# Kernel tuning notes

Hardware: AMD Instinct MI355X
Metric: run time of the kernel (lower is better)

## Reference

```python
import jax, jax.numpy as jnp
import numpy as np

H = 512; W = 512; C = 32; B = 2; N = 120000; HEADS = 2; HD = C // HEADS; S = 9
INDEX_SHIFT = jnp.array([[0,0],[-1,0],[1,0],[0,1],[-1,1],[1,1],[0,-1],[-1,-1],[1,-1]], dtype=jnp.int32)


def setup_inputs() -> dict:
    key = jax.random.key(0)
    ks = jax.random.split(key, 20)
    bev_feats = jax.random.normal(ks[0], (B, N, C), jnp.float32)
    coors = []
    for b in range(B):
        perm = jax.random.permutation(ks[1 + b], H * W)[:N]
        coors.append(jnp.stack([perm // W, perm % W], axis=-1))
    bev_coors = jnp.stack(coors).astype(jnp.int32)
    s = 1.0 / np.sqrt(C)
    u = lambda k, shape, lim: jax.random.uniform(k, shape, jnp.float32, -lim, lim)
    return {
        'bev_feats': bev_feats,
        'bev_coors': bev_coors,
        'ln_w': jnp.ones((C,), jnp.float32),
        'ln_b': jnp.zeros((C,), jnp.float32),
        'wq': u(ks[3], (C, C), s), 'bq': u(ks[4], (C,), s),
        'wk': u(ks[5], (C, C), s), 'bk': u(ks[6], (C,), s),
        'wv': u(ks[7], (C, C), s), 'bv': u(ks[8], (C,), s),
        'pos_w': u(ks[9], (C, 2), 1.0 / np.sqrt(2.0)), 'pos_b': u(ks[10], (C,), 1.0 / np.sqrt(2.0)),
        'in_w': u(ks[11], (3 * C, C), s), 'in_b': jnp.zeros((3 * C,), jnp.float32),
        'out_w': u(ks[12], (C, C), s), 'out_b': jnp.zeros((C,), jnp.float32),
    }


def reference(bev_feats, bev_coors, ln_w, ln_b, wq, bq, wk, bk, wv, bv, pos_w, pos_b, in_w, in_b, out_w, out_b):
    def single(feats, coors):
        # LayerNorm (biased var, eps=1e-5)
        mu = feats.mean(-1, keepdims=True)
        var = feats.var(-1, keepdims=True)
        x = (feats - mu) / jnp.sqrt(var + 1e-5) * ln_w + ln_b
        # qkv 1x1 conv == linear
        q = x @ wq.T + bq
        k = x @ wk.T + bk
        v = x @ wv.T + bv
        # dense grid lookup: coord -> voxel index (-1 if empty)
        flat0 = coors[:, 0] * W + coors[:, 1]
        grid = jnp.full((H * W,), -1, jnp.int32).at[flat0].set(jnp.arange(N, dtype=jnp.int32))
        sc = coors[None] + INDEX_SHIFT[:, None]                      # [9,N,2]
        valid = (sc[..., 0] >= 0) & (sc[..., 0] < H) & (sc[..., 1] >= 0) & (sc[..., 1] < W)
        flat = jnp.clip(sc[..., 0], 0, H - 1) * W + jnp.clip(sc[..., 1], 0, W - 1)
        idx = jnp.where(valid, grid[flat], -1)                       # [9,N]
        pos = INDEX_SHIFT.astype(x.dtype) @ pos_w.T + pos_b          # [9,C]
        m = (idx >= 0)[..., None]
        tv = jnp.where(m, v[idx] + pos[:, None, :], 0.0)             # [9,N,C]
        tk = jnp.where(m, k[idx], 0.0)
        keyt = jnp.swapaxes(tk, 0, 1)                                # [N,9,C]
        valt = jnp.swapaxes(tv, 0, 1)
        # tiny MHA: query len 1, kv len 9, 2 heads (dropout inactive at eval)
        qp = q @ in_w[:C].T + in_b[:C]
        kp = keyt @ in_w[C:2 * C].T + in_b[C:2 * C]
        vp = valt @ in_w[2 * C:].T + in_b[2 * C:]
        qh = qp.reshape(N, HEADS, HD)
        kh = kp.reshape(N, S, HEADS, HD)
        vh = vp.reshape(N, S, HEADS, HD)
        attn = jax.nn.softmax(jnp.einsum('nhd,nshd->nhs', qh, kh) / np.sqrt(HD), axis=-1)
        o = jnp.einsum('nhs,nshd->nhd', attn, vh).reshape(N, C)
        o = o @ out_w.T + out_b
        # scatter to pseudo image [C,H,W]
        canvas = jnp.zeros((C, H * W), o.dtype).at[:, flat0].set(o.T)
        return canvas.reshape(C, H, W)
    return jax.vmap(single)(bev_feats, bev_coors)
```

## Files before the change

kernel.cpp:

```cpp
#include <hip/hip_runtime.h>
#include <hip/hip_fp16.h>
#include <cstdio>
#include <cstdint>

#define HH 512
#define WW 512
#define CC 32
#define BB 2
#define NN 120000
#define HWPIX (HH*WW)
#define NPTS (BB*NN)
#define NPIX (BB*HWPIX)
#define NBLK (NPIX/256)

__device__ __forceinline__ void h8_to_f8(float4 raw, float* o) {
    const __half2* h = (const __half2*)&raw;
    #pragma unroll
    for (int i = 0; i < 4; ++i) {
        float2 f = __half22float2(h[i]);
        o[2 * i] = f.x; o[2 * i + 1] = f.y;
    }
}

__global__ __launch_bounds__(256) void prep(const float* __restrict__ wq, const float* __restrict__ wk,
                          const float* __restrict__ wv, const float* __restrict__ in_w,
                          const float* __restrict__ out_w,
                          const float* __restrict__ bq, const float* __restrict__ bk,
                          const float* __restrict__ bv, const float* __restrict__ in_b,
                          const float* __restrict__ pos_w, const float* __restrict__ pos_b,
                          float* __restrict__ M, float* __restrict__ V, int* __restrict__ cnt) {
    int blk = blockIdx.x;
    if (blk < 16) {
        int tid = blk * 256 + threadIdx.x;
        int which = tid >> 10;
        int e = tid & 1023;
        int cp = e & 31;
        int j  = e >> 5;
        if (which < 3) {
            const float* w = (which == 0) ? wq : ((which == 1) ? wk : wv);
            const float* Wrow = in_w + (which * 32 + cp) * 32;
            float acc = 0.f;
            #pragma unroll
            for (int t = 0; t < 32; ++t) acc += Wrow[t] * w[t * 32 + j];
            M[which * 1024 + j * 32 + cp] = acc;
        } else {
            M[3 * 1024 + j * 32 + cp] = out_w[cp * 32 + j];
        }
    } else if (blk == 16) {
        int tid = threadIdx.x;
        if (tid < 32) {
            float a = 0.f, b = 0.f, c = 0.f;
            #pragma unroll
            for (int t = 0; t < 32; ++t) {
                a += in_w[tid * 32 + t] * bq[t];
                b += in_w[(32 + tid) * 32 + t] * bk[t];
                c += in_w[(64 + tid) * 32 + t] * bv[t];
            }
            V[tid]      = a + in_b[tid];
            V[32 + tid] = b;
            V[64 + tid] = c;
        } else if (tid < 128) {
            int grp = (tid - 32) >> 5;
            int cp  = tid & 31;
            float acc = 0.f;
            #pragma unroll
            for (int t = 0; t < 32; ++t) {
                float src = (grp == 0) ? pos_w[t * 2 + 0] : ((grp == 1) ? pos_w[t * 2 + 1] : pos_b[t]);
                acc += in_w[(64 + cp) * 32 + t] * src;
            }
            V[96 + grp * 32 + cp] = acc;
        }
    } else {
        for (int i = threadIdx.x; i < 2048; i += 256) cnt[i] = 0;
    }
}

__global__ void build_grid(const int* __restrict__ coors, int* __restrict__ grid,
                           int* __restrict__ cnt) {
    int P = blockIdx.x * blockDim.x + threadIdx.x;
    if (P >= NPTS) return;
    int b = P / NN;
    int n = P - b * NN;
    int y = coors[P * 2 + 0];
    int x = coors[P * 2 + 1];
    int pix = b * HWPIX + y * WW + x;
    grid[pix] = n;
    atomicAdd(&cnt[pix >> 8], 1);
}

__global__ __launch_bounds__(256) void scan2048(const int* __restrict__ cnt, int* __restrict__ off) {
    __shared__ int ps[256];
    int tid = threadIdx.x;
    int v[8], loc[8];
    int t = 0;
    #pragma unroll
    for (int k = 0; k < 8; ++k) { v[k] = cnt[tid * 8 + k]; loc[k] = t; t += v[k]; }
    ps[tid] = t;
    __syncthreads();
    for (int d = 1; d < 256; d <<= 1) {
        int val = ps[tid];
        int add = (tid >= d) ? ps[tid - d] : 0;
        __syncthreads();
        ps[tid] = val + add;
        __syncthreads();
    }
    int excl = (tid > 0) ? ps[tid - 1] : 0;
    #pragma unroll
    for (int k = 0; k < 8; ++k) off[tid * 8 + k] = excl + loc[k];
}

__global__ __launch_bounds__(256) void assign_ranks(const int* __restrict__ off,
                                                    int* __restrict__ grid,
                                                    int* __restrict__ rmap,
                                                    int* __restrict__ plist) {
    __shared__ int woff[4];
    int tid = threadIdx.x;
    int pix = blockIdx.x * 256 + tid;
    int n = grid[pix];
    bool occ = n >= 0;
    unsigned long long mask = __ballot(occ);
    int lane = tid & 63, wvi = tid >> 6;
    if (lane == 0) woff[wvi] = __popcll(mask);
    __syncthreads();
    int pre = 0;
    for (int w = 0; w < wvi; ++w) pre += woff[w];
    if (occ) {
        int r = off[blockIdx.x] + pre + __popcll(mask & ((1ull << lane) - 1ull));
        grid[pix] = r;
        rmap[(pix >> 18) * NN + n] = r;
        plist[r] = pix;
    }
}

__global__ __launch_bounds__(256) void stage1(const float* __restrict__ feats,
                                              const float* __restrict__ ln_w,
                                              const float* __restrict__ ln_b,
                                              const float* __restrict__ M,
                                              const float* __restrict__ V,
                                              const int* __restrict__ rmap,
                                              float* __restrict__ qp,
                                              __half* __restrict__ kvh) {
    int gp = blockIdx.x * 256 + threadIdx.x;
    if (gp >= NPTS) return;
    int r = rmap[gp];

    const float* fr = feats + ((size_t)gp << 5);
    float x[32];
    #pragma unroll
    for (int k = 0; k < 8; ++k) ((float4*)x)[k] = ((const float4*)fr)[k];

    float s1 = 0.f, s2 = 0.f;
    #pragma unroll
    for (int j = 0; j < 32; ++j) { s1 += x[j]; s2 += x[j] * x[j]; }
    float mu   = s1 * (1.f / 32.f);
    float var  = s2 * (1.f / 32.f) - mu * mu;
    float rstd = rsqrtf(var + 1e-5f);
    #pragma unroll
    for (int j = 0; j < 32; ++j) x[j] = (x[j] - mu) * rstd * ln_w[j] + ln_b[j];

    float acc[32];

    #pragma unroll
    for (int c = 0; c < 32; ++c) acc[c] = V[c];
    #pragma unroll
    for (int j = 0; j < 32; ++j) {
        float xv = x[j];
        #pragma unroll
        for (int c = 0; c < 32; ++c) acc[c] += xv * M[j * 32 + c];
    }
    {
        float4* qd = (float4*)(qp + ((size_t)r << 5));
        #pragma unroll
        for (int k = 0; k < 8; ++k) qd[k] = ((float4*)acc)[k];
    }

    __half2 kvbuf[32];

    #pragma unroll
    for (int c = 0; c < 32; ++c) acc[c] = V[32 + c];
    #pragma unroll
    for (int j = 0; j < 32; ++j) {
        float xv = x[j];
        #pragma unroll
        for (int c = 0; c < 32; ++c) acc[c] += xv * M[1024 + j * 32 + c];
    }
    #pragma unroll
    for (int c = 0; c < 16; ++c) kvbuf[c] = __floats2half2_rn(acc[2 * c], acc[2 * c + 1]);

    #pragma unroll
    for (int c = 0; c < 32; ++c) acc[c] = V[64 + c];
    #pragma unroll
    for (int j = 0; j < 32; ++j) {
        float xv = x[j];
        #pragma unroll
        for (int c = 0; c < 32; ++c) acc[c] += xv * M[2048 + j * 32 + c];
    }
    #pragma unroll
    for (int c = 0; c < 16; ++c) kvbuf[16 + c] = __floats2half2_rn(acc[2 * c], acc[2 * c + 1]);

    float4* kd = (float4*)(kvh + ((size_t)r << 6));
    #pragma unroll
    for (int k = 0; k < 8; ++k) kd[k] = ((float4*)kvbuf)[k];
}

__global__ __launch_bounds__(256) void stage2(const int* __restrict__ grid,
                                              const int* __restrict__ plist,
                                              const __half* __restrict__ kvh,
                                              const float* __restrict__ M,
                                              const float* __restrict__ V,
                                              const float* __restrict__ in_b,
                                              const float* __restrict__ out_b,
                                              const float* __restrict__ qp,
                                              __half* __restrict__ obuf) {
    __shared__ float lsf[256 * 18];

    int w = (blockIdx.x & 7) * 118 + (blockIdx.x >> 3);
    if (w >= 938) return;
    int tid = threadIdx.x;
    int r0 = w * 256;
    int r = r0 + tid;
    int rc = (r < NPTS) ? r : (NPTS - 1);

    int pix = plist[rc];
    int b = pix >> 18;
    int p = pix & (HWPIX - 1);
    int y = p >> 9, x = p & 511;

    const int DYC[9] = {0,-1,1,0,-1,1,0,-1,1};
    const int DXC[9] = {0,0,0,1,1,1,-1,-1,-1};

    float qf[32];
    {
        const float4* q4 = (const float4*)(qp + ((size_t)rc << 5));
        #pragma unroll
        for (int k = 0; k < 8; ++k) ((float4*)qf)[k] = q4[k];
    }

    int nr[9];
    #pragma unroll
    for (int s = 0; s < 9; ++s) {
        int sy = y + DYC[s], sx = x + DXC[s];
        nr[s] = (sy >= 0 && sy < HH && sx >= 0 && sx < WW) ? grid[(b << 18) + (sy << 9) + sx] : -1;
    }

    float eb0 = 0.f, eb1 = 0.f;
    #pragma unroll
    for (int i = 0; i < 16; ++i) {
        eb0 += qf[i]      * in_b[32 + i];
        eb1 += qf[16 + i] * in_b[48 + i];
    }

    float lg0[9], lg1[9];
    #pragma unroll
    for (int s = 0; s < 9; ++s) {
        float d0 = eb0, d1 = eb1;
        if (nr[s] >= 0) {
            const float4* kp = (const float4*)(kvh + ((size_t)nr[s] << 6));
            float kf[32];
            h8_to_f8(kp[0], kf);      h8_to_f8(kp[1], kf + 8);
            h8_to_f8(kp[2], kf + 16); h8_to_f8(kp[3], kf + 24);
            #pragma unroll
            for (int i = 0; i < 16; ++i) {
                d0 += qf[i]      * kf[i];
                d1 += qf[16 + i] * kf[16 + i];
            }
        }
        lg0[s] = d0 * 0.25f;
        lg1[s] = d1 * 0.25f;
    }
    float m0 = lg0[0], m1 = lg1[0];
    #pragma unroll
    for (int s = 1; s < 9; ++s) { m0 = fmaxf(m0, lg0[s]); m1 = fmaxf(m1, lg1[s]); }
    float l0 = 0.f, l1 = 0.f;
    #pragma unroll
    for (int s = 0; s < 9; ++s) {
        lg0[s] = __expf(lg0[s] - m0); l0 += lg0[s];
        lg1[s] = __expf(lg1[s] - m1); l1 += lg1[s];
    }

    float o[32];
    #pragma unroll
    for (int i = 0; i < 32; ++i) o[i] = 0.f;
    float wdy0 = 0.f, wdx0 = 0.f, woc0 = 0.f;
    float wdy1 = 0.f, wdx1 = 0.f, woc1 = 0.f;
    #pragma unroll
    for (int s = 0; s < 9; ++s) {
        if (nr[s] >= 0) {
            float w0 = lg0[s], w1 = lg1[s];
            const float4* vp = (const float4*)(kvh + ((size_t)nr[s] << 6)) + 4;
            float vf[32];
            h8_to_f8(vp[0], vf);      h8_to_f8(vp[1], vf + 8);
            h8_to_f8(vp[2], vf + 16); h8_to_f8(vp[3], vf + 24);
            #pragma unroll
            for (int i = 0; i < 16; ++i) {
                o[i]      += w0 * vf[i];
                o[16 + i] += w1 * vf[16 + i];
            }
            wdy0 += w0 * (float)DYC[s]; wdx0 += w0 * (float)DXC[s]; woc0 += w0;
            wdy1 += w1 * (float)DYC[s]; wdx1 += w1 * (float)DXC[s]; woc1 += w1;
        }
    }
    float rl0 = 1.f / l0, rl1 = 1.f / l1;
    #pragma unroll
    for (int i = 0; i < 16; ++i) {
        o[i]      = (o[i]      + wdy0 * V[96 + i]      + wdx0 * V[128 + i]      + woc0 * V[160 + i])      * rl0 + in_b[64 + i];
        o[16 + i] = (o[16 + i] + wdy1 * V[96 + 16 + i] + wdx1 * V[128 + 16 + i] + woc1 * V[160 + 16 + i]) * rl1 + in_b[80 + i];
    }

    float acc[32];
    #pragma unroll
    for (int c = 0; c < 32; ++c) acc[c] = out_b[c];
    #pragma unroll
    for (int j = 0; j < 32; ++j) {
        float vj = o[j];
        #pragma unroll
        for (int c = 0; c < 32; ++c) acc[c] += vj * M[3072 + j * 32 + c];
    }

    {
        float hbuf[16];
        __half2* hp = (__half2*)hbuf;
        #pragma unroll
        for (int c = 0; c < 16; ++c) hp[c] = __floats2half2_rn(acc[2 * c], acc[2 * c + 1]);
        float* lrow = lsf + tid * 18;
        #pragma unroll
        for (int j = 0; j < 8; ++j) *(float2*)(lrow + j * 2) = ((float2*)hbuf)[j];
    }
    __syncthreads();

    #pragma unroll
    for (int k = 0; k < 8; ++k) {
        int ii  = k * 32 + (tid >> 3);
        int col = tid & 7;
        if (r0 + ii < NPTS) {
            float2 val = *(const float2*)(lsf + ii * 18 + col * 2);
            *(float2*)(obuf + ((size_t)(r0 + ii) << 5) + col * 4) = val;
        }
    }
}

__global__ __launch_bounds__(256) void stage3(const int* __restrict__ grid,
                                              const __half* __restrict__ obuf,
                                              float* __restrict__ out) {
    int w = (blockIdx.x & 7) * 256 + (blockIdx.x >> 3);
    int t = w * 256 + threadIdx.x;
    int b = t >> 18;
    int p = t & (HWPIX - 1);
    int rk = grid[t];
    float r[32];
    if (rk >= 0) {
        const float4* row = (const float4*)(obuf + ((size_t)rk << 5));
        float4 raw0 = row[0], raw1 = row[1], raw2 = row[2], raw3 = row[3];
        h8_to_f8(raw0, r); h8_to_f8(raw1, r + 8); h8_to_f8(raw2, r + 16); h8_to_f8(raw3, r + 24);
    } else {
        #pragma unroll
        for (int i = 0; i < 32; ++i) r[i] = 0.f;
    }
    float* outb = out + (size_t)b * CC * HWPIX + p;
    #pragma unroll
    for (int cc = 0; cc < 32; ++cc) outb[cc * HWPIX] = r[cc];
}

extern "C" void kernel_launch(void* const* d_in, const int* in_sizes, int n_in,
                              void* d_out, int out_size, void* d_ws, size_t ws_size,
                              hipStream_t stream) {
    const float* feats = (const float*)d_in[0];
    const int*   coors = (const int*)d_in[1];
    const float* ln_w  = (const float*)d_in[2];
    const float* ln_b  = (const float*)d_in[3];
    const float* wq    = (const float*)d_in[4];
    const float* bq    = (const float*)d_in[5];
    const float* wk    = (const float*)d_in[6];
    const float* bk    = (const float*)d_in[7];
    const float* wv    = (const float*)d_in[8];
    const float* bv    = (const float*)d_in[9];
    const float* pos_w = (const float*)d_in[10];
    const float* pos_b = (const float*)d_in[11];
    const float* in_w  = (const float*)d_in[12];
    const float* in_b  = (const float*)d_in[13];
    const float* out_w = (const float*)d_in[14];
    const float* out_b = (const float*)d_in[15];

    int*    grid = (int*)d_ws;
    float*  qp   = (float*)d_ws + NPIX;
    __half* kvh  = (__half*)(qp + (size_t)NPTS * 32);
    __half* obuf = kvh + (size_t)NPTS * 64;
    float*  M    = (float*)(obuf + (size_t)NPTS * 32);
    float*  V    = M + 4096;
    size_t need = ((size_t)NPIX + (size_t)NPTS * 32 + (size_t)NPTS * 16
                   + (size_t)NPTS * 8 + 4096 + 192) * sizeof(float);
    if (ws_size < need) {
        fprintf(stderr, "kernel_launch: ws too small: %zu < %zu\n", ws_size, need);
        return;
    }
    int* cnt   = (int*)d_out + (out_size - 4096);
    int* off   = cnt + 2048;
    int* rmap  = (int*)d_out + (out_size - 4096 - 2 * NPTS);
    int* plist = rmap + NPTS;

    hipMemsetAsync(grid, 0xFF, (size_t)NPIX * sizeof(int), stream);
    prep<<<18, 256, 0, stream>>>(wq, wk, wv, in_w, out_w, bq, bk, bv, in_b, pos_w, pos_b, M, V, cnt);
    build_grid<<<(NPTS + 255) / 256, 256, 0, stream>>>(coors, grid, cnt);
    scan2048<<<1, 256, 0, stream>>>(cnt, off);
    assign_ranks<<<NBLK, 256, 0, stream>>>(off, grid, rmap, plist);
    stage1<<<(NPTS + 255) / 256, 256, 0, stream>>>(feats, ln_w, ln_b, M, V, rmap, qp, kvh);
    stage2<<<944, 256, 0, stream>>>(grid, plist, kvh, M, V, in_b, out_b, qp, obuf);
    stage3<<<NBLK, 256, 0, stream>>>(grid, obuf, (float*)d_out);
}
```

Before: 236.8 us.

## Fuse attention and canvas scatter into one pixel-block kernel with fp16 queries

Merges the attention stage and the canvas-writing stage into one kernel that walks 256-pixel blocks. Each block compacts its occupied pixels in shared memory, runs the attention for them, and writes the whole output tile directly. This removes the obuf round trip and the plist array. Queries are now stored as fp16 instead of fp32, which halves that traffic but loses precision. stage1 also moves to 128-thread blocks with no bounds check. The cost is that blocks with few occupied pixels leave many threads idle during the attention math.

```diff
diff --git a/kernel.cpp b/kernel.cpp
--- a/kernel.cpp
+++ b/kernel.cpp
@@ -111,8 +111,7 @@
 
 __global__ __launch_bounds__(256) void assign_ranks(const int* __restrict__ off,
                                                     int* __restrict__ grid,
-                                                    int* __restrict__ rmap,
-                                                    int* __restrict__ plist) {
+                                                    int* __restrict__ rmap) {
     __shared__ int woff[4];
     int tid = threadIdx.x;
     int pix = blockIdx.x * 256 + tid;
@@ -128,20 +127,18 @@
         int r = off[blockIdx.x] + pre + __popcll(mask & ((1ull << lane) - 1ull));
         grid[pix] = r;
         rmap[(pix >> 18) * NN + n] = r;
-        plist[r] = pix;
-    }
-}
-
-__global__ __launch_bounds__(256) void stage1(const float* __restrict__ feats,
+    }
+}
+
+__global__ __launch_bounds__(128) void stage1(const float* __restrict__ feats,
                                               const float* __restrict__ ln_w,
                                               const float* __restrict__ ln_b,
                                               const float* __restrict__ M,
                                               const float* __restrict__ V,
                                               const int* __restrict__ rmap,
-                                              float* __restrict__ qp,
+                                              __half* __restrict__ qh,
                                               __half* __restrict__ kvh) {
-    int gp = blockIdx.x * 256 + threadIdx.x;
-    if (gp >= NPTS) return;
+    int gp = blockIdx.x * 128 + threadIdx.x;
     int r = rmap[gp];
 
     const float* fr = feats + ((size_t)gp << 5);
@@ -159,6 +156,7 @@
     for (int j = 0; j < 32; ++j) x[j] = (x[j] - mu) * rstd * ln_w[j] + ln_b[j];
 
     float acc[32];
+    __half2 hbuf[16];
 
     #pragma unroll
     for (int c = 0; c < 32; ++c) acc[c] = V[c];
@@ -168,10 +166,12 @@
         #pragma unroll
         for (int c = 0; c < 32; ++c) acc[c] += xv * M[j * 32 + c];
     }
+    #pragma unroll
+    for (int c = 0; c < 16; ++c) hbuf[c] = __floats2half2_rn(acc[2 * c], acc[2 * c + 1]);
     {
-        float4* qd = (float4*)(qp + ((size_t)r << 5));
-        #pragma unroll
-        for (int k = 0; k < 8; ++k) qd[k] = ((float4*)acc)[k];
+        float4* qd = (float4*)(qh + ((size_t)r << 5));
+        #pragma unroll
+        for (int k = 0; k < 4; ++k) qd[k] = ((float4*)hbuf)[k];
     }
 
     __half2 kvbuf[32];
@@ -203,162 +203,159 @@
     for (int k = 0; k < 8; ++k) kd[k] = ((float4*)kvbuf)[k];
 }
 
-__global__ __launch_bounds__(256) void stage2(const int* __restrict__ grid,
-                                              const int* __restrict__ plist,
-                                              const __half* __restrict__ kvh,
-                                              const float* __restrict__ M,
-                                              const float* __restrict__ V,
-                                              const float* __restrict__ in_b,
-                                              const float* __restrict__ out_b,
-                                              const float* __restrict__ qp,
-                                              __half* __restrict__ obuf) {
-    __shared__ float lsf[256 * 18];
-
-    int w = (blockIdx.x & 7) * 118 + (blockIdx.x >> 3);
-    if (w >= 938) return;
+__global__ __launch_bounds__(256) void stage23(const int* __restrict__ grid,
+                                               const __half* __restrict__ qh,
+                                               const __half* __restrict__ kvh,
+                                               const float* __restrict__ M,
+                                               const float* __restrict__ V,
+                                               const float* __restrict__ in_b,
+                                               const float* __restrict__ out_b,
+                                               float* __restrict__ out) {
+    __shared__ __half2 lso[256 * 17];
+    __shared__ int lsr[256], lsp[256];
+    __shared__ int woff[4];
+
+    int w = (blockIdx.x & 7) * 256 + (blockIdx.x >> 3);
     int tid = threadIdx.x;
-    int r0 = w * 256;
-    int r = r0 + tid;
-    int rc = (r < NPTS) ? r : (NPTS - 1);
-
-    int pix = plist[rc];
+    int pix = w * 256 + tid;
+
+    int rk = grid[pix];
+    bool occ = rk >= 0;
+    unsigned long long mask = __ballot(occ);
+    int lane = tid & 63, wvi = tid >> 6;
+    if (lane == 0) woff[wvi] = __popcll(mask);
+    __syncthreads();
+    int pre = 0;
+    for (int ww = 0; ww < wvi; ++ww) pre += woff[ww];
+    int cnt = woff[0] + woff[1] + woff[2] + woff[3];
+    int slot = -1;
+    if (occ) {
+        slot = pre + __popcll(mask & ((1ull << lane) - 1ull));
+        lsr[slot] = rk;
+        lsp[slot] = tid;
+    }
+    __syncthreads();
+
+    const int DYC[9] = {0,-1,1,0,-1,1,0,-1,1};
+    const int DXC[9] = {0,0,0,1,1,1,-1,-1,-1};
+
+    if (tid < cnt) {
+        int i = tid;
+        int r = lsr[i];
+        int pixl = w * 256 + lsp[i];
+        int b = pixl >> 18;
+        int p = pixl & (HWPIX - 1);
+        int y = p >> 9, x = p & 511;
+
+        float qf[32];
+        {
+            const float4* q4 = (const float4*)(qh + ((size_t)r << 5));
+            float4 r0 = q4[0], r1 = q4[1], r2 = q4[2], r3 = q4[3];
+            h8_to_f8(r0, qf); h8_to_f8(r1, qf + 8); h8_to_f8(r2, qf + 16); h8_to_f8(r3, qf + 24);
+        }
+
+        int nr[9];
+        #pragma unroll
+        for (int s = 0; s < 9; ++s) {
+            int sy = y + DYC[s], sx = x + DXC[s];
+            nr[s] = (sy >= 0 && sy < HH && sx >= 0 && sx < WW) ? grid[(b << 18) + (sy << 9) + sx] : -1;
+        }
+
+        float eb0 = 0.f, eb1 = 0.f;
+        #pragma unroll
+        for (int c = 0; c < 16; ++c) {
+            eb0 += qf[c]      * in_b[32 + c];
+            eb1 += qf[16 + c] * in_b[48 + c];
+        }
+
+        float lg0[9], lg1[9];
+        #pragma unroll
+        for (int s = 0; s < 9; ++s) {
+            float d0 = eb0, d1 = eb1;
+            if (nr[s] >= 0) {
+                const float4* kp = (const float4*)(kvh + ((size_t)nr[s] << 6));
+                float kf[32];
+                h8_to_f8(kp[0], kf);      h8_to_f8(kp[1], kf + 8);
+                h8_to_f8(kp[2], kf + 16); h8_to_f8(kp[3], kf + 24);
+                #pragma unroll
+                for (int c = 0; c < 16; ++c) {
+                    d0 += qf[c]      * kf[c];
+                    d1 += qf[16 + c] * kf[16 + c];
+                }
+            }
+            lg0[s] = d0 * 0.25f;
+            lg1[s] = d1 * 0.25f;
+        }
+        float m0 = lg0[0], m1 = lg1[0];
+        #pragma unroll
+        for (int s = 1; s < 9; ++s) { m0 = fmaxf(m0, lg0[s]); m1 = fmaxf(m1, lg1[s]); }
+        float l0 = 0.f, l1 = 0.f;
+        #pragma unroll
+        for (int s = 0; s < 9; ++s) {
+            lg0[s] = __expf(lg0[s] - m0); l0 += lg0[s];
+            lg1[s] = __expf(lg1[s] - m1); l1 += lg1[s];
+        }
+
+        float o[32];
+        #pragma unroll
+        for (int c = 0; c < 32; ++c) o[c] = 0.f;
+        float wdy0 = 0.f, wdx0 = 0.f, woc0 = 0.f;
+        float wdy1 = 0.f, wdx1 = 0.f, woc1 = 0.f;
+        #pragma unroll
+        for (int s = 0; s < 9; ++s) {
+            if (nr[s] >= 0) {
+                float w0 = lg0[s], w1 = lg1[s];
+                const float4* vp = (const float4*)(kvh + ((size_t)nr[s] << 6)) + 4;
+                float vf[32];
+                h8_to_f8(vp[0], vf);      h8_to_f8(vp[1], vf + 8);
+                h8_to_f8(vp[2], vf + 16); h8_to_f8(vp[3], vf + 24);
+                #pragma unroll
+                for (int c = 0; c < 16; ++c) {
+                    o[c]      += w0 * vf[c];
+                    o[16 + c] += w1 * vf[16 + c];
+                }
+                wdy0 += w0 * (float)DYC[s]; wdx0 += w0 * (float)DXC[s]; woc0 += w0;
+                wdy1 += w1 * (float)DYC[s]; wdx1 += w1 * (float)DXC[s]; woc1 += w1;
+            }
+        }
+        float rl0 = 1.f / l0, rl1 = 1.f / l1;
+        #pragma unroll
+        for (int c = 0; c < 16; ++c) {
+            o[c]      = (o[c]      + wdy0 * V[96 + c]      + wdx0 * V[128 + c]      + woc0 * V[160 + c])      * rl0 + in_b[64 + c];
+            o[16 + c] = (o[16 + c] + wdy1 * V[96 + 16 + c] + wdx1 * V[128 + 16 + c] + woc1 * V[160 + 16 + c]) * rl1 + in_b[80 + c];
+        }
+
+        float acc[32];
+        #pragma unroll
+        for (int c = 0; c < 32; ++c) acc[c] = out_b[c];
+        #pragma unroll
+        for (int j = 0; j < 32; ++j) {
+            float vj = o[j];
+            #pragma unroll
+            for (int c = 0; c < 32; ++c) acc[c] += vj * M[3072 + j * 32 + c];
+        }
+
+        __half2* lrow = lso + i * 17;
+        #pragma unroll
+        for (int c = 0; c < 16; ++c) lrow[c] = __floats2half2_rn(acc[2 * c], acc[2 * c + 1]);
+    }
+    __syncthreads();
+
     int b = pix >> 18;
     int p = pix & (HWPIX - 1);
-    int y = p >> 9, x = p & 511;
-
-    const int DYC[9] = {0,-1,1,0,-1,1,0,-1,1};
-    const int DXC[9] = {0,0,0,1,1,1,-1,-1,-1};
-
-    float qf[32];
-    {
-        const float4* q4 = (const float4*)(qp + ((size_t)rc << 5));
-        #pragma unroll
-        for (int k = 0; k < 8; ++k) ((float4*)qf)[k] = q4[k];
-    }
-
-    int nr[9];
-    #pragma unroll
-    for (int s = 0; s < 9; ++s) {
-        int sy = y + DYC[s], sx = x + DXC[s];
-        nr[s] = (sy >= 0 && sy < HH && sx >= 0 && sx < WW) ? grid[(b << 18) + (sy << 9) + sx] : -1;
-    }
-
-    float eb0 = 0.f, eb1 = 0.f;
-    #pragma unroll
-    for (int i = 0; i < 16; ++i) {
-        eb0 += qf[i]      * in_b[32 + i];
-        eb1 += qf[16 + i] * in_b[48 + i];
-    }
-
-    float lg0[9], lg1[9];
-    #pragma unroll
-    for (int s = 0; s < 9; ++s) {
-        float d0 = eb0, d1 = eb1;
-        if (nr[s] >= 0) {
-            const float4* kp = (const float4*)(kvh + ((size_t)nr[s] << 6));
-            float kf[32];
-            h8_to_f8(kp[0], kf);      h8_to_f8(kp[1], kf + 8);
-            h8_to_f8(kp[2], kf + 16); h8_to_f8(kp[3], kf + 24);
-            #pragma unroll
-            for (int i = 0; i < 16; ++i) {
-                d0 += qf[i]      * kf[i];
-                d1 += qf[16 + i] * kf[16 + i];
-            }
-        }
-        lg0[s] = d0 * 0.25f;
-        lg1[s] = d1 * 0.25f;
-    }
-    float m0 = lg0[0], m1 = lg1[0];
-    #pragma unroll
-    for (int s = 1; s < 9; ++s) { m0 = fmaxf(m0, lg0[s]); m1 = fmaxf(m1, lg1[s]); }
-    float l0 = 0.f, l1 = 0.f;
-    #pragma unroll
-    for (int s = 0; s < 9; ++s) {
-        lg0[s] = __expf(lg0[s] - m0); l0 += lg0[s];
-        lg1[s] = __expf(lg1[s] - m1); l1 += lg1[s];
-    }
-
-    float o[32];
-    #pragma unroll
-    for (int i = 0; i < 32; ++i) o[i] = 0.f;
-    float wdy0 = 0.f, wdx0 = 0.f, woc0 = 0.f;
-    float wdy1 = 0.f, wdx1 = 0.f, woc1 = 0.f;
-    #pragma unroll
-    for (int s = 0; s < 9; ++s) {
-        if (nr[s] >= 0) {
-            float w0 = lg0[s], w1 = lg1[s];
-            const float4* vp = (const float4*)(kvh + ((size_t)nr[s] << 6)) + 4;
-            float vf[32];
-            h8_to_f8(vp[0], vf);      h8_to_f8(vp[1], vf + 8);
-            h8_to_f8(vp[2], vf + 16); h8_to_f8(vp[3], vf + 24);
-            #pragma unroll
-            for (int i = 0; i < 16; ++i) {
-                o[i]      += w0 * vf[i];
-                o[16 + i] += w1 * vf[16 + i];
-            }
-            wdy0 += w0 * (float)DYC[s]; wdx0 += w0 * (float)DXC[s]; woc0 += w0;
-            wdy1 += w1 * (float)DYC[s]; wdx1 += w1 * (float)DXC[s]; woc1 += w1;
-        }
-    }
-    float rl0 = 1.f / l0, rl1 = 1.f / l1;
-    #pragma unroll
-    for (int i = 0; i < 16; ++i) {
-        o[i]      = (o[i]      + wdy0 * V[96 + i]      + wdx0 * V[128 + i]      + woc0 * V[160 + i])      * rl0 + in_b[64 + i];
-        o[16 + i] = (o[16 + i] + wdy1 * V[96 + 16 + i] + wdx1 * V[128 + 16 + i] + woc1 * V[160 + 16 + i]) * rl1 + in_b[80 + i];
-    }
-
-    float acc[32];
-    #pragma unroll
-    for (int c = 0; c < 32; ++c) acc[c] = out_b[c];
-    #pragma unroll
-    for (int j = 0; j < 32; ++j) {
-        float vj = o[j];
-        #pragma unroll
-        for (int c = 0; c < 32; ++c) acc[c] += vj * M[3072 + j * 32 + c];
-    }
-
-    {
-        float hbuf[16];
-        __half2* hp = (__half2*)hbuf;
-        #pragma unroll
-        for (int c = 0; c < 16; ++c) hp[c] = __floats2half2_rn(acc[2 * c], acc[2 * c + 1]);
-        float* lrow = lsf + tid * 18;
-        #pragma unroll
-        for (int j = 0; j < 8; ++j) *(float2*)(lrow + j * 2) = ((float2*)hbuf)[j];
-    }
-    __syncthreads();
-
-    #pragma unroll
-    for (int k = 0; k < 8; ++k) {
-        int ii  = k * 32 + (tid >> 3);
-        int col = tid & 7;
-        if (r0 + ii < NPTS) {
-            float2 val = *(const float2*)(lsf + ii * 18 + col * 2);
-            *(float2*)(obuf + ((size_t)(r0 + ii) << 5) + col * 4) = val;
-        }
-    }
-}
-
-__global__ __launch_bounds__(256) void stage3(const int* __restrict__ grid,
-                                              const __half* __restrict__ obuf,
-                                              float* __restrict__ out) {
-    int w = (blockIdx.x & 7) * 256 + (blockIdx.x >> 3);
-    int t = w * 256 + threadIdx.x;
-    int b = t >> 18;
-    int p = t & (HWPIX - 1);
-    int rk = grid[t];
-    float r[32];
-    if (rk >= 0) {
-        const float4* row = (const float4*)(obuf + ((size_t)rk << 5));
-        float4 raw0 = row[0], raw1 = row[1], raw2 = row[2], raw3 = row[3];
-        h8_to_f8(raw0, r); h8_to_f8(raw1, r + 8); h8_to_f8(raw2, r + 16); h8_to_f8(raw3, r + 24);
+    float* outb = out + (size_t)b * CC * HWPIX + p;
+    if (occ) {
+        const __half2* lrow = lso + slot * 17;
+        #pragma unroll
+        for (int c2 = 0; c2 < 16; ++c2) {
+            float2 f = __half22float2(lrow[c2]);
+            outb[(2 * c2) * HWPIX]     = f.x;
+            outb[(2 * c2 + 1) * HWPIX] = f.y;
+        }
     } else {
         #pragma unroll
-        for (int i = 0; i < 32; ++i) r[i] = 0.f;
-    }
-    float* outb = out + (size_t)b * CC * HWPIX + p;
-    #pragma unroll
-    for (int cc = 0; cc < 32; ++cc) outb[cc * HWPIX] = r[cc];
+        for (int cc = 0; cc < 32; ++cc) outb[cc * HWPIX] = 0.f;
+    }
 }
 
 extern "C" void kernel_launch(void* const* d_in, const int* in_sizes, int n_in,
@@ -382,28 +379,24 @@
     const float* out_b = (const float*)d_in[15];
 
     int*    grid = (int*)d_ws;
-    float*  qp   = (float*)d_ws + NPIX;
-    __half* kvh  = (__half*)(qp + (size_t)NPTS * 32);
-    __half* obuf = kvh + (size_t)NPTS * 64;
-    float*  M    = (float*)(obuf + (size_t)NPTS * 32);
+    __half* qh   = (__half*)((int*)d_ws + NPIX);
+    __half* kvh  = qh + (size_t)NPTS * 32;
+    float*  M    = (float*)(kvh + (size_t)NPTS * 64);
     float*  V    = M + 4096;
-    size_t need = ((size_t)NPIX + (size_t)NPTS * 32 + (size_t)NPTS * 16
-                   + (size_t)NPTS * 8 + 4096 + 192) * sizeof(float);
+    size_t need = (size_t)NPIX * 4 + (size_t)NPTS * 96 * 2 + (4096 + 192) * 4;
     if (ws_size < need) {
         fprintf(stderr, "kernel_launch: ws too small: %zu < %zu\n", ws_size, need);
         return;
     }
-    int* cnt   = (int*)d_out + (out_size - 4096);
-    int* off   = cnt + 2048;
-    int* rmap  = (int*)d_out + (out_size - 4096 - 2 * NPTS);
-    int* plist = rmap + NPTS;
+    int* cnt  = (int*)d_out + (out_size - 4096);
+    int* off  = cnt + 2048;
+    int* rmap = (int*)d_out + (out_size - 4096 - NPTS);
 
     hipMemsetAsync(grid, 0xFF, (size_t)NPIX * sizeof(int), stream);
     prep<<<18, 256, 0, stream>>>(wq, wk, wv, in_w, out_w, bq, bk, bv, in_b, pos_w, pos_b, M, V, cnt);
     build_grid<<<(NPTS + 255) / 256, 256, 0, stream>>>(coors, grid, cnt);
     scan2048<<<1, 256, 0, stream>>>(cnt, off);
-    assign_ranks<<<NBLK, 256, 0, stream>>>(off, grid, rmap, plist);
-    stage1<<<(NPTS + 255) / 256, 256, 0, stream>>>(feats, ln_w, ln_b, M, V, rmap, qp, kvh);
-    stage2<<<944, 256, 0, stream>>>(grid, plist, kvh, M, V, in_b, out_b, qp, obuf);
-    stage3<<<NBLK, 256, 0, stream>>>(grid, obuf, (float*)d_out);
-}
+    assign_ranks<<<NBLK, 256, 0, stream>>>(off, grid, rmap);
+    stage1<<<NPTS / 128, 128, 0, stream>>>(feats, ln_w, ln_b, M, V, rmap, qh, kvh);
+    stage23<<<NBLK, 256, 0, stream>>>(grid, qh, kvh, M, V, in_b, out_b, (float*)d_out);
+}
```

Measured after the change: 237.1 us. About the same (+0.1%).
